# Kernel tuning notes

Measured on AMD Instinct MI355X. Metric: run time of the kernel, lower is better.

The kernel has to match this reference:

```python
import jax, jax.numpy as jnp
import numpy as np

D = 1024

def setup_inputs() -> dict:
    key = jax.random.key(0)
    ks = jax.random.split(key, 7)
    s = 1.0 / np.sqrt(D)  # torch Linear default init scale (uniform bound)
    x = jax.random.normal(ks[0], (4, 2048, D), dtype=jnp.float32)
    Wq = jax.random.uniform(ks[1], (D, D), jnp.float32, -s, s)
    Wk = jax.random.uniform(ks[2], (D, D), jnp.float32, -s, s)
    Wv = jax.random.uniform(ks[3], (D, D), jnp.float32, -s, s)
    bq = jax.random.uniform(ks[4], (D,), jnp.float32, -s, s)
    bk = jax.random.uniform(ks[5], (D,), jnp.float32, -s, s)
    bv = jax.random.uniform(ks[6], (D,), jnp.float32, -s, s)
    return {"x": x, "Wq": Wq, "bq": bq, "Wk": Wk, "bk": bk, "Wv": Wv, "bv": bv}

def reference(x, Wq, bq, Wk, bk, Wv, bv):
    # Linear layers: y = x @ W^T + b (weights stored torch-style [out, in])
    Q = jnp.einsum('bsd,ed->bse', x, Wq) + bq
    K = jnp.einsum('bsd,ed->bse', x, Wk) + bk
    V = jnp.einsum('bsd,ed->bse', x, Wv) + bv
    scale = jnp.sqrt(jnp.asarray(Q.shape[-1], Q.dtype))
    scores = jnp.einsum('bqd,bkd->bqk', Q, K) / scale  # [B, S, S]
    probs = jax.nn.softmax(scores, axis=-1)
    return jnp.einsum('bqk,bkd->bqd', probs, V)
```

## Files before the change

kernel.cpp:

```cpp
#include <hip/hip_runtime.h>


typedef __bf16 bf16x8 __attribute__((ext_vector_type(8)));
typedef float f32x4 __attribute__((ext_vector_type(4)));
typedef unsigned short u16;

__device__ __forceinline__ u16 f2b(float f) {
  union { float f; unsigned u; } a; a.f = f;
  unsigned r = a.u + 0x7fffu + ((a.u >> 16) & 1u);
  return (u16)(r >> 16);
}

__global__ __launch_bounds__(256) void cast_x_kernel(const float* __restrict__ in,
                                                     u16* __restrict__ out, int n4) {
  int i = blockIdx.x * 256 + threadIdx.x;
  if (i < n4) {
    float4 v = reinterpret_cast<const float4*>(in)[i];
    reinterpret_cast<ushort4*>(out)[i] =
        make_ushort4(f2b(v.x), f2b(v.y), f2b(v.z), f2b(v.w));
  }
}

__global__ __launch_bounds__(256) void cast_w_kernel(const float* __restrict__ Wq,
                                                     const float* __restrict__ Wk,
                                                     const float* __restrict__ Wv,
                                                     u16* __restrict__ out) {
  const int b = blockIdx.x;
  const int w = b >> 10;
  const float* src = (w == 0) ? Wq : (w == 1) ? Wk : Wv;
  const int i = (b & 1023) * 256 + threadIdx.x;
  float4 v = reinterpret_cast<const float4*>(src)[i];
  reinterpret_cast<ushort4*>(out + (size_t)w * 1048576)[i] =
      make_ushort4(f2b(v.x), f2b(v.y), f2b(v.z), f2b(v.w));
}

template <int GEOM, int NT>
__device__ __forceinline__ void core8(const char* __restrict__ Ab,
                                      const char* __restrict__ Bb, int lda, int ldb,
                                      char* smem, f32x4* acc) {
  constexpr int LDSBUF = GEOM ? 49152 : 65536;
  constexpr int BOFF = GEOM ? 16384 : 32768;
  constexpr int AHALF = GEOM ? 8192 : 16384;
  const int tid = threadIdx.x;
  const int wave = tid >> 6, lane = tid & 63;
  const int wr = wave >> 2, wc = wave & 3;
  const int fr = lane & 15, fg = lane >> 4;
  const int rd = (fr * 64 + fg * 16) ^ (((fr >> 3) & 1) << 5);
  const int li = (lane * 16) ^ ((lane >> 5) << 5);
  const int sr = li >> 6, sc2 = li & 63;

  auto STAGE = [&](int kt, int p) {
    const int isB = p & 1, s = p >> 1;
    char* lds = smem + (kt & 1) * LDSBUF + (isB ? BOFF + s * 16384 : s * AHALF);
    const char* gb = isB ? Bb : Ab;
    const int ldx = isB ? ldb : lda;
    const int colOff = kt * 128 + s * 64 + sc2;
    __builtin_amdgcn_global_load_lds(
        (const __attribute__((address_space(1))) void*)(gb + (size_t)(wave * 16 + sr) * ldx + colOff),
        (__attribute__((address_space(3))) void*)(lds + wave * 1024), 16, 0, 0);
    if (isB || GEOM == 0)
      __builtin_amdgcn_global_load_lds(
          (const __attribute__((address_space(1))) void*)(gb + (size_t)((8 + wave) * 16 + sr) * ldx + colOff),
          (__attribute__((address_space(3))) void*)(lds + 8192 + wave * 1024), 16, 0, 0);
  };

#pragma unroll
  for (int p = 0; p < 4; ++p) STAGE(0, p);
  if constexpr (GEOM == 0) asm volatile("s_waitcnt vmcnt(4)" ::: "memory");
  else asm volatile("s_waitcnt vmcnt(3)" ::: "memory");
  __builtin_amdgcn_s_barrier();
  __builtin_amdgcn_sched_barrier(0);

  bf16x8 keep[4];
  for (int kt = 0; kt < NT; ++kt) {
    const char* bufA = smem + (kt & 1) * LDSBUF;
    const char* bufB = bufA + BOFF;
    const bool notlast = (kt + 1 < NT);
#pragma unroll
    for (int p = 0; p < 4; ++p) {
      const int s = p >> 1, j = p & 1;
      if constexpr (GEOM == 0) {
        bf16x8 afr[4];
        if (j == 0)
#pragma unroll
          for (int n = 0; n < 4; ++n)
            keep[n] = *reinterpret_cast<const bf16x8*>(bufB + s * 16384 + (wc * 4 + n) * 1024 + rd);
#pragma unroll
        for (int m = 0; m < 4; ++m)
          afr[m] = *reinterpret_cast<const bf16x8*>(bufA + s * 16384 + (wr * 8 + j * 4 + m) * 1024 + rd);
        if (notlast) STAGE(kt + 1, p);
        __builtin_amdgcn_s_barrier();
        __builtin_amdgcn_sched_barrier(0);
        __builtin_amdgcn_s_setprio(1);
#pragma unroll
        for (int m = 0; m < 4; ++m)
#pragma unroll
          for (int n = 0; n < 4; ++n)
            acc[(j * 4 + m) * 4 + n] = __builtin_amdgcn_mfma_f32_16x16x32_bf16(
                afr[m], keep[n], acc[(j * 4 + m) * 4 + n], 0, 0, 0);
        __builtin_amdgcn_s_setprio(0);
      } else {
        bf16x8 bfr[2];
        if (j == 0)
#pragma unroll
          for (int m = 0; m < 4; ++m)
            keep[m] = *reinterpret_cast<const bf16x8*>(bufA + s * AHALF + (wr * 4 + m) * 1024 + rd);
#pragma unroll
        for (int nn = 0; nn < 2; ++nn)
          bfr[nn] = *reinterpret_cast<const bf16x8*>(bufB + s * 16384 + (wc * 4 + j * 2 + nn) * 1024 + rd);
        if (notlast) STAGE(kt + 1, p);
        __builtin_amdgcn_s_barrier();
        __builtin_amdgcn_sched_barrier(0);
        __builtin_amdgcn_s_setprio(1);
#pragma unroll
        for (int m = 0; m < 4; ++m)
#pragma unroll
          for (int nn = 0; nn < 2; ++nn)
            acc[m * 4 + j * 2 + nn] = __builtin_amdgcn_mfma_f32_16x16x32_bf16(
                keep[m], bfr[nn], acc[m * 4 + j * 2 + nn], 0, 0, 0);
        __builtin_amdgcn_s_setprio(0);
      }
      if (p == 1 || p == 3) {
        if (notlast) {
          if constexpr (GEOM == 0) asm volatile("s_waitcnt vmcnt(4)" ::: "memory");
          else asm volatile("s_waitcnt vmcnt(3)" ::: "memory");
        } else {
          asm volatile("s_waitcnt vmcnt(0)" ::: "memory");
        }
      }
      __builtin_amdgcn_s_barrier();
      __builtin_amdgcn_sched_barrier(0);
    }
  }
}

__global__ __launch_bounds__(512, 2) void proj8_kernel(
    const u16* __restrict__ A, const u16* __restrict__ Bm,
    const float* __restrict__ bq, const float* __restrict__ bk,
    const float* __restrict__ bvv, u16* __restrict__ QK, u16* __restrict__ Vt) {
  extern __shared__ char smem[];
  constexpr int NT = 16;
  const int tid = threadIdx.x;
  const int wave = tid >> 6, lane = tid & 63;
  const int wr = wave >> 2, wc = wave & 3;
  const int tileM = blockIdx.x * 256;
  const int tileN = blockIdx.y * 256;
  const int fr = lane & 15, fg = lane >> 4;
  const int rd_inner = (fr * 64 + fg * 16) ^ (((fr >> 3) & 1) << 5);
  const int li = (lane * 16) ^ ((lane >> 5) << 5);
  const int sr = li >> 6, sc2 = li & 63;
  const int rowA0 = wave * 16 + sr;
  const int rowA1 = 128 + wave * 16 + sr;
  const char* Ab = (const char*)A + (size_t)tileM * 2048;
  const char* Bb = (const char*)Bm + (size_t)tileN * 2048;

  auto STAGE = [&](int kt, int p) {
    const int isB = p & 1, s = p >> 1;
    char* ldsHalf = smem + (kt & 1) * 65536 + isB * 32768 + s * 16384;
    const char* gb = isB ? Bb : Ab;
    const int colOff = kt * 128 + s * 64;
    const char* g0 = gb + (size_t)rowA0 * 2048 + colOff + sc2;
    const char* g1 = gb + (size_t)rowA1 * 2048 + colOff + sc2;
    __builtin_amdgcn_global_load_lds(
        (const __attribute__((address_space(1))) void*)g0,
        (__attribute__((address_space(3))) void*)(ldsHalf + wave * 1024), 16, 0, 0);
    __builtin_amdgcn_global_load_lds(
        (const __attribute__((address_space(1))) void*)g1,
        (__attribute__((address_space(3))) void*)(ldsHalf + 8192 + wave * 1024), 16, 0, 0);
  };

#pragma unroll
  for (int p = 0; p < 4; ++p) STAGE(0, p);
  asm volatile("s_waitcnt vmcnt(4)" ::: "memory");
  __builtin_amdgcn_s_barrier();
  __builtin_amdgcn_sched_barrier(0);

  f32x4 acc[8][4] = {};
  bf16x8 bfr[4];

  for (int kt = 0; kt < NT; ++kt) {
    const char* bufA = smem + (kt & 1) * 65536;
    const char* bufB = bufA + 32768;
    const bool notlast = (kt + 1 < NT);
#pragma unroll
    for (int p = 0; p < 4; ++p) {
      const int s = p >> 1, j = p & 1;
      bf16x8 afr[4];
      if (j == 0) {
#pragma unroll
        for (int n = 0; n < 4; ++n)
          bfr[n] = *reinterpret_cast<const bf16x8*>(bufB + s * 16384 +
                                                    (wc * 4 + n) * 1024 + rd_inner);
      }
#pragma unroll
      for (int m = 0; m < 4; ++m)
        afr[m] = *reinterpret_cast<const bf16x8*>(bufA + s * 16384 +
                                                  (wr * 8 + j * 4 + m) * 1024 + rd_inner);
      if (notlast) STAGE(kt + 1, p);
      __builtin_amdgcn_s_barrier();
      __builtin_amdgcn_sched_barrier(0);
      __builtin_amdgcn_s_setprio(1);
#pragma unroll
      for (int m = 0; m < 4; ++m)
#pragma unroll
        for (int n = 0; n < 4; ++n)
          acc[j * 4 + m][n] = __builtin_amdgcn_mfma_f32_16x16x32_bf16(
              afr[m], bfr[n], acc[j * 4 + m][n], 0, 0, 0);
      __builtin_amdgcn_s_setprio(0);
      if (p == 1 || p == 3) {
        if (notlast) asm volatile("s_waitcnt vmcnt(4)" ::: "memory");
        else asm volatile("s_waitcnt vmcnt(0)" ::: "memory");
      }
      __builtin_amdgcn_s_barrier();
      __builtin_amdgcn_sched_barrier(0);
    }
  }

  const int w = blockIdx.y >> 2;
  const float* bias = (w == 0) ? bq : (w == 1) ? bk : bvv;
  if (w < 2) {
    u16* O = QK + (size_t)w * 8388608;
#pragma unroll
    for (int mi = 0; mi < 8; ++mi) {
      const int r0 = tileM + wr * 128 + mi * 16 + fg * 4;
#pragma unroll
      for (int n = 0; n < 4; ++n) {
        const int cw = (tileN + wc * 64 + n * 16 + fr) & 1023;
        const float bi = bias[cw];
#pragma unroll
        for (int jj = 0; jj < 4; ++jj)
          O[(size_t)(r0 + jj) * 1024 + cw] = f2b(acc[mi][n][jj] + bi);
      }
    }
  } else {
#pragma unroll
    for (int mi = 0; mi < 8; ++mi) {
      const int r0 = tileM + wr * 128 + mi * 16 + fg * 4;
      const int b = r0 >> 11, s0 = r0 & 2047;
#pragma unroll
      for (int n = 0; n < 4; ++n) {
        const int cw = (tileN + wc * 64 + n * 16 + fr) & 1023;
        const float bi = bias[cw];
        ushort4 u = make_ushort4(f2b(acc[mi][n][0] + bi), f2b(acc[mi][n][1] + bi),
                                 f2b(acc[mi][n][2] + bi), f2b(acc[mi][n][3] + bi));
        *reinterpret_cast<ushort4*>(&Vt[(size_t)b * 2097152 + (size_t)cw * 2048 + s0]) = u;
      }
    }
  }
}

__global__ __launch_bounds__(512, 2) void sc8_kernel(const u16* __restrict__ Qb,
                                                     const u16* __restrict__ Kb,
                                                     u16* __restrict__ P,
                                                     float* __restrict__ rowpart) {
  extern __shared__ char smem[];
  const int z = blockIdx.z;
  const int tileM = blockIdx.x * 256, tileN = blockIdx.y * 256;
  f32x4 acc[32] = {};
  core8<0, 16>((const char*)Qb + (size_t)z * 4194304 + (size_t)tileM * 2048,
               (const char*)Kb + (size_t)z * 4194304 + (size_t)tileN * 2048, 2048, 2048,
               smem, acc);
  const int tid = threadIdx.x;
  const int wave = tid >> 6, lane = tid & 63;
  const int wr = wave >> 2, wc = wave & 3, fr = lane & 15, fg = lane >> 4;
  float* rs = (float*)smem;
  u16* Po = P + (size_t)z * 4194304 + (size_t)tileM * 2048 + tileN;
#pragma unroll
  for (int mi = 0; mi < 8; ++mi) {
#pragma unroll
    for (int jj = 0; jj < 4; ++jj) {
      const int rl = wr * 128 + mi * 16 + fg * 4 + jj;
      float part = 0.f;
#pragma unroll
      for (int n = 0; n < 4; ++n) {
        float e = __expf(acc[mi * 4 + n][jj] * 0.03125f);
        part += e;
        Po[(size_t)rl * 2048 + wc * 64 + n * 16 + fr] = f2b(e);
      }
      part += __shfl_xor(part, 1);
      part += __shfl_xor(part, 2);
      part += __shfl_xor(part, 4);
      part += __shfl_xor(part, 8);
      if (fr == 0) rs[wc * 256 + rl] = part;
    }
  }
  __syncthreads();
  if (tid < 256) {
    float s = rs[tid] + rs[256 + tid] + rs[512 + tid] + rs[768 + tid];
    rowpart[(size_t)blockIdx.y * 8192 + z * 2048 + tileM + tid] = s;
  }
}

__global__ __launch_bounds__(256) void rsum_kernel(const float* __restrict__ rowpart,
                                                   float* __restrict__ rowinv) {
  const int i = blockIdx.x * 256 + threadIdx.x;
  float s = 0.f;
#pragma unroll
  for (int t = 0; t < 8; ++t) s += rowpart[t * 8192 + i];
  rowinv[i] = 1.0f / s;
}

__global__ __launch_bounds__(512, 2) void pv8_kernel(const u16* __restrict__ P,
                                                     const u16* __restrict__ Vt,
                                                     const float* __restrict__ rowinv,
                                                     float* __restrict__ out) {
  extern __shared__ char smem[];
  const int z = blockIdx.z;
  const int tileM = blockIdx.x * 128, tileN = blockIdx.y * 256;
  f32x4 acc[16] = {};
  core8<1, 32>((const char*)P + (size_t)z * 8388608 + (size_t)tileM * 4096,
               (const char*)Vt + (size_t)z * 4194304 + (size_t)tileN * 4096, 4096, 4096,
               smem, acc);
  const int tid = threadIdx.x;
  const int wave = tid >> 6, lane = tid & 63;
  const int wr = wave >> 2, wc = wave & 3, fr = lane & 15, fg = lane >> 4;
  float* O = out + (size_t)z * 2097152;
  const float* ri = rowinv + z * 2048 + tileM;
#pragma unroll
  for (int mi = 0; mi < 4; ++mi) {
#pragma unroll
    for (int jj = 0; jj < 4; ++jj) {
      const int r = wr * 64 + mi * 16 + fg * 4 + jj;
      const float inv = ri[r];
#pragma unroll
      for (int n = 0; n < 4; ++n)
        O[(size_t)(tileM + r) * 1024 + tileN + wc * 64 + n * 16 + fr] =
            acc[mi * 4 + n][jj] * inv;
    }
  }
}

extern "C" void kernel_launch(void* const* d_in, const int* in_sizes, int n_in,
                              void* d_out, int out_size, void* d_ws, size_t ws_size,
                              hipStream_t stream) {
  if (ws_size < ((size_t)72 << 20)) return;
  const float* x = (const float*)d_in[0];
  const float* Wq = (const float*)d_in[1];
  const float* bq = (const float*)d_in[2];
  const float* Wk = (const float*)d_in[3];
  const float* bk = (const float*)d_in[4];
  const float* Wv = (const float*)d_in[5];
  const float* bv = (const float*)d_in[6];
  char* ws = (char*)d_ws;
  u16* xb = (u16*)(ws);
  u16* Pb = (u16*)(ws);
  u16* Qb = (u16*)(ws + ((size_t)16 << 20));
  u16* Kb = (u16*)(ws + ((size_t)32 << 20));
  u16* Vt = (u16*)(ws + ((size_t)48 << 20));
  u16* Wb = (u16*)(ws + ((size_t)64 << 20));
  float* rowpart = (float*)(ws + ((size_t)70 << 20));
  float* rowinv = (float*)(ws + ((size_t)70 << 20) + 262144);
  float* out = (float*)d_out;

  (void)hipFuncSetAttribute((const void*)proj8_kernel,
                            hipFuncAttributeMaxDynamicSharedMemorySize, 131072);
  (void)hipFuncSetAttribute((const void*)sc8_kernel,
                            hipFuncAttributeMaxDynamicSharedMemorySize, 131072);
  (void)hipFuncSetAttribute((const void*)pv8_kernel,
                            hipFuncAttributeMaxDynamicSharedMemorySize, 98304);

  cast_x_kernel<<<8192, 256, 0, stream>>>(x, xb, 2097152);
  cast_w_kernel<<<3072, 256, 0, stream>>>(Wq, Wk, Wv, Wb);

  proj8_kernel<<<dim3(32, 12), 512, 131072, stream>>>(xb, Wb, bq, bk, bv, Qb, Vt);

  sc8_kernel<<<dim3(8, 8, 4), 512, 131072, stream>>>(Qb, Kb, Pb, rowpart);
  rsum_kernel<<<32, 256, 0, stream>>>(rowpart, rowinv);
  pv8_kernel<<<dim3(16, 4, 4), 512, 98304, stream>>>(Pb, Vt, rowinv, out);
}
```

Measured before the change: 161.9 us.

## Deepen GEMM prefetch pipeline and reuse core8 in projection kernel

The shared core8 GEMM loop now issues the loads for the second half of the next-next k-tile early, keeping more global-to-LDS loads in flight with adjusted vmcnt waits. The second half of each buffer is refilled as soon as it has been consumed, so more load latency is hidden behind MFMA work. The projection kernel drops its duplicated GEMM loop and calls core8, so it gets the same deeper pipeline. The risk is buffer-reuse hazards: the vmcnt counts and barrier placement must exactly match the new load ordering.

```diff
diff --git a/kernel.cpp b/kernel.cpp
--- a/kernel.cpp
+++ b/kernel.cpp
@@ -66,8 +66,10 @@
 
 #pragma unroll
   for (int p = 0; p < 4; ++p) STAGE(0, p);
-  if constexpr (GEOM == 0) asm volatile("s_waitcnt vmcnt(4)" ::: "memory");
-  else asm volatile("s_waitcnt vmcnt(3)" ::: "memory");
+  STAGE(1, 0);
+  STAGE(1, 1);
+  if constexpr (GEOM == 0) asm volatile("s_waitcnt vmcnt(8)" ::: "memory");
+  else asm volatile("s_waitcnt vmcnt(6)" ::: "memory");
   __builtin_amdgcn_s_barrier();
   __builtin_amdgcn_sched_barrier(0);
 
@@ -75,7 +77,6 @@
   for (int kt = 0; kt < NT; ++kt) {
     const char* bufA = smem + (kt & 1) * LDSBUF;
     const char* bufB = bufA + BOFF;
-    const bool notlast = (kt + 1 < NT);
 #pragma unroll
     for (int p = 0; p < 4; ++p) {
       const int s = p >> 1, j = p & 1;
@@ -88,7 +89,8 @@
 #pragma unroll
         for (int m = 0; m < 4; ++m)
           afr[m] = *reinterpret_cast<const bf16x8*>(bufA + s * 16384 + (wr * 8 + j * 4 + m) * 1024 + rd);
-        if (notlast) STAGE(kt + 1, p);
+        if (p < 2) { if (kt + 1 < NT) STAGE(kt + 1, p + 2); }
+        else       { if (kt + 2 < NT) STAGE(kt + 2, p - 2); }
         __builtin_amdgcn_s_barrier();
         __builtin_amdgcn_sched_barrier(0);
         __builtin_amdgcn_s_setprio(1);
@@ -108,7 +110,8 @@
 #pragma unroll
         for (int nn = 0; nn < 2; ++nn)
           bfr[nn] = *reinterpret_cast<const bf16x8*>(bufB + s * 16384 + (wc * 4 + j * 2 + nn) * 1024 + rd);
-        if (notlast) STAGE(kt + 1, p);
+        if (p < 2) { if (kt + 1 < NT) STAGE(kt + 1, p + 2); }
+        else       { if (kt + 2 < NT) STAGE(kt + 2, p - 2); }
         __builtin_amdgcn_s_barrier();
         __builtin_amdgcn_sched_barrier(0);
         __builtin_amdgcn_s_setprio(1);
@@ -120,12 +123,20 @@
                 keep[m], bfr[nn], acc[m * 4 + j * 2 + nn], 0, 0, 0);
         __builtin_amdgcn_s_setprio(0);
       }
-      if (p == 1 || p == 3) {
-        if (notlast) {
+      if (p == 1) {
+        if (kt < NT - 1) {
+          if constexpr (GEOM == 0) asm volatile("s_waitcnt vmcnt(8)" ::: "memory");
+          else asm volatile("s_waitcnt vmcnt(6)" ::: "memory");
+        } else {
+          asm volatile("s_waitcnt vmcnt(0)" ::: "memory");
+        }
+      } else if (p == 3) {
+        if (kt < NT - 2) {
+          if constexpr (GEOM == 0) asm volatile("s_waitcnt vmcnt(8)" ::: "memory");
+          else asm volatile("s_waitcnt vmcnt(6)" ::: "memory");
+        } else if (kt == NT - 2) {
           if constexpr (GEOM == 0) asm volatile("s_waitcnt vmcnt(4)" ::: "memory");
           else asm volatile("s_waitcnt vmcnt(3)" ::: "memory");
-        } else {
-          asm volatile("s_waitcnt vmcnt(0)" ::: "memory");
         }
       }
       __builtin_amdgcn_s_barrier();
@@ -139,83 +150,13 @@
     const float* __restrict__ bq, const float* __restrict__ bk,
     const float* __restrict__ bvv, u16* __restrict__ QK, u16* __restrict__ Vt) {
   extern __shared__ char smem[];
-  constexpr int NT = 16;
+  const int tileM = blockIdx.x * 256, tileN = blockIdx.y * 256;
+  f32x4 acc[32] = {};
+  core8<0, 16>((const char*)A + (size_t)tileM * 2048,
+               (const char*)Bm + (size_t)tileN * 2048, 2048, 2048, smem, acc);
   const int tid = threadIdx.x;
   const int wave = tid >> 6, lane = tid & 63;
-  const int wr = wave >> 2, wc = wave & 3;
-  const int tileM = blockIdx.x * 256;
-  const int tileN = blockIdx.y * 256;
-  const int fr = lane & 15, fg = lane >> 4;
-  const int rd_inner = (fr * 64 + fg * 16) ^ (((fr >> 3) & 1) << 5);
-  const int li = (lane * 16) ^ ((lane >> 5) << 5);
-  const int sr = li >> 6, sc2 = li & 63;
-  const int rowA0 = wave * 16 + sr;
-  const int rowA1 = 128 + wave * 16 + sr;
-  const char* Ab = (const char*)A + (size_t)tileM * 2048;
-  const char* Bb = (const char*)Bm + (size_t)tileN * 2048;
-
-  auto STAGE = [&](int kt, int p) {
-    const int isB = p & 1, s = p >> 1;
-    char* ldsHalf = smem + (kt & 1) * 65536 + isB * 32768 + s * 16384;
-    const char* gb = isB ? Bb : Ab;
-    const int colOff = kt * 128 + s * 64;
-    const char* g0 = gb + (size_t)rowA0 * 2048 + colOff + sc2;
-    const char* g1 = gb + (size_t)rowA1 * 2048 + colOff + sc2;
-    __builtin_amdgcn_global_load_lds(
-        (const __attribute__((address_space(1))) void*)g0,
-        (__attribute__((address_space(3))) void*)(ldsHalf + wave * 1024), 16, 0, 0);
-    __builtin_amdgcn_global_load_lds(
-        (const __attribute__((address_space(1))) void*)g1,
-        (__attribute__((address_space(3))) void*)(ldsHalf + 8192 + wave * 1024), 16, 0, 0);
-  };
-
-#pragma unroll
-  for (int p = 0; p < 4; ++p) STAGE(0, p);
-  asm volatile("s_waitcnt vmcnt(4)" ::: "memory");
-  __builtin_amdgcn_s_barrier();
-  __builtin_amdgcn_sched_barrier(0);
-
-  f32x4 acc[8][4] = {};
-  bf16x8 bfr[4];
-
-  for (int kt = 0; kt < NT; ++kt) {
-    const char* bufA = smem + (kt & 1) * 65536;
-    const char* bufB = bufA + 32768;
-    const bool notlast = (kt + 1 < NT);
-#pragma unroll
-    for (int p = 0; p < 4; ++p) {
-      const int s = p >> 1, j = p & 1;
-      bf16x8 afr[4];
-      if (j == 0) {
-#pragma unroll
-        for (int n = 0; n < 4; ++n)
-          bfr[n] = *reinterpret_cast<const bf16x8*>(bufB + s * 16384 +
-                                                    (wc * 4 + n) * 1024 + rd_inner);
-      }
-#pragma unroll
-      for (int m = 0; m < 4; ++m)
-        afr[m] = *reinterpret_cast<const bf16x8*>(bufA + s * 16384 +
-                                                  (wr * 8 + j * 4 + m) * 1024 + rd_inner);
-      if (notlast) STAGE(kt + 1, p);
-      __builtin_amdgcn_s_barrier();
-      __builtin_amdgcn_sched_barrier(0);
-      __builtin_amdgcn_s_setprio(1);
-#pragma unroll
-      for (int m = 0; m < 4; ++m)
-#pragma unroll
-        for (int n = 0; n < 4; ++n)
-          acc[j * 4 + m][n] = __builtin_amdgcn_mfma_f32_16x16x32_bf16(
-              afr[m], bfr[n], acc[j * 4 + m][n], 0, 0, 0);
-      __builtin_amdgcn_s_setprio(0);
-      if (p == 1 || p == 3) {
-        if (notlast) asm volatile("s_waitcnt vmcnt(4)" ::: "memory");
-        else asm volatile("s_waitcnt vmcnt(0)" ::: "memory");
-      }
-      __builtin_amdgcn_s_barrier();
-      __builtin_amdgcn_sched_barrier(0);
-    }
-  }
-
+  const int wr = wave >> 2, wc = wave & 3, fr = lane & 15, fg = lane >> 4;
   const int w = blockIdx.y >> 2;
   const float* bias = (w == 0) ? bq : (w == 1) ? bk : bvv;
   if (w < 2) {
@@ -229,7 +170,7 @@
         const float bi = bias[cw];
 #pragma unroll
         for (int jj = 0; jj < 4; ++jj)
-          O[(size_t)(r0 + jj) * 1024 + cw] = f2b(acc[mi][n][jj] + bi);
+          O[(size_t)(r0 + jj) * 1024 + cw] = f2b(acc[mi * 4 + n][jj] + bi);
       }
     }
   } else {
@@ -241,8 +182,8 @@
       for (int n = 0; n < 4; ++n) {
         const int cw = (tileN + wc * 64 + n * 16 + fr) & 1023;
         const float bi = bias[cw];
-        ushort4 u = make_ushort4(f2b(acc[mi][n][0] + bi), f2b(acc[mi][n][1] + bi),
-                                 f2b(acc[mi][n][2] + bi), f2b(acc[mi][n][3] + bi));
+        ushort4 u = make_ushort4(f2b(acc[mi * 4 + n][0] + bi), f2b(acc[mi * 4 + n][1] + bi),
+                                 f2b(acc[mi * 4 + n][2] + bi), f2b(acc[mi * 4 + n][3] + bi));
         *reinterpret_cast<ushort4*>(&Vt[(size_t)b * 2097152 + (size_t)cw * 2048 + s0]) = u;
       }
     }
```

New measurement: 160.8 us. Within noise of the previous version (-0.7%).
